# Performance work log

Hardware: AMD Instinct MI355X
Metric: run time of the kernel (lower is better)

Reference implementation:

```python
import jax, jax.numpy as jnp
import numpy as np

GROUP_SIZE = 128  # infeatures // n_groups = 4096 // 32


def setup_inputs() -> dict:
    key = jax.random.key(0)
    k1, k2, k3, k4 = jax.random.split(key, 4)
    M, K, N = 256, 4096, 4096
    n_groups = K // GROUP_SIZE  # 32
    A = jax.random.normal(k1, (M, K), dtype=jnp.float32)
    # uint4 quantized weights, stored unpacked as int32 in [0, 16)
    qweight = jax.random.randint(k2, (N, K), 0, 16, dtype=jnp.int32)
    scales = jax.random.uniform(k3, (N, n_groups), dtype=jnp.float32) * 0.05 + 1e-3
    zeros = jax.random.uniform(k4, (N, n_groups), dtype=jnp.float32) * 15.0
    return {"A": A, "qweight": qweight, "scales": scales, "zeros": zeros}


def reference(A, qweight, scales, zeros):
    # Fused dequant + GEMM: W[n,k] = (q[n,k] - zeros[n, k//G]) * scales[n, k//G]
    N, K = qweight.shape
    s = jnp.repeat(scales, GROUP_SIZE, axis=1)   # [N, K]
    z = jnp.repeat(zeros, GROUP_SIZE, axis=1)    # [N, K]
    W = (qweight.astype(A.dtype) - z) * s        # dequantized weight [N, K]
    # Linear: Y = A @ W^T  -> [M, N]
    return jnp.einsum('mk,nk->mn', A, W)
```

## Files before the change

### kernel.cpp

```cpp
#include <hip/hip_runtime.h>

typedef __attribute__((ext_vector_type(8))) short bf16x8;
typedef __attribute__((ext_vector_type(4))) float f32x4;

#define MDIM 256
#define NDIM 4096
#define KDIM 4096
#define NGRP 32
#define BM 128
#define BN 32
#define BK 64
#define NT (KDIM / BK)

typedef const __attribute__((address_space(1))) void* gas_ptr;
typedef __attribute__((address_space(3))) void* las_ptr;

__device__ __forceinline__ unsigned short f2bf(float f) {
  union { float f; unsigned int u; } v;
  v.f = f;
  unsigned int r = v.u + 0x7FFFu + ((v.u >> 16) & 1u);
  return (unsigned short)(r >> 16);
}

__device__ __forceinline__ void gl_lds16(const void* g, void* l) {
  __builtin_amdgcn_global_load_lds((gas_ptr)g, (las_ptr)l, 16, 0, 0);
}

__global__ void convA_kernel(const float* __restrict__ A,
                             unsigned short* __restrict__ Ab) {
  int i = blockIdx.x * 256 + threadIdx.x;
  float4 v = reinterpret_cast<const float4*>(A)[i];
  ushort4 o;
  o.x = f2bf(v.x); o.y = f2bf(v.y); o.z = f2bf(v.z); o.w = f2bf(v.w);
  reinterpret_cast<ushort4*>(Ab)[i] = o;
}

__global__ __launch_bounds__(256, 1) void gemm_kernel(
    const unsigned short* __restrict__ Ab, const int* __restrict__ qw,
    const float* __restrict__ sc, const float* __restrict__ zr,
    float* __restrict__ out) {
  __shared__ __align__(16) unsigned short A_lds[4][BM * BK];
  __shared__ __align__(16) unsigned short W_lds[2][BN * BK];
  __shared__ float s_lds[BN * NGRP];
  __shared__ float zs_lds[BN * NGRP];

  const int tid = threadIdx.x;
  const int lane = tid & 63;
  const int wave = tid >> 6;
  const int wm = wave >> 1;
  const int wn = wave & 1;

  const int bid = blockIdx.x;
  const int swz = (bid & 7) * 32 + (bid >> 3);
  const int m0 = (swz & 1) * BM;
  const int n0 = (swz >> 1) * BN;

  for (int i = tid; i < BN * NGRP; i += 256) {
    int n = i >> 5;
    int g = i & 31;
    float s = sc[(size_t)(n0 + n) * NGRP + g];
    float z = zr[(size_t)(n0 + n) * NGRP + g];
    s_lds[i] = s;
    zs_lds[i] = z * s;
  }

  const unsigned short* Abase = Ab + (size_t)m0 * KDIM;
  const int wrow = tid >> 3;
  const int wc = tid & 7;
  const int* qbase = qw + (size_t)(n0 + wrow) * KDIM + wc * 8;

  int4 qr[4][2];

  auto loadW = [&](int t, int idx) {
    const int* p = qbase + t * BK;
    qr[idx][0] = *reinterpret_cast<const int4*>(p);
    qr[idx][1] = *reinterpret_cast<const int4*>(p + 4);
  };
  auto stageA = [&](int t, int b) {
#pragma unroll
    for (int i = 0; i < 4; ++i) {
      int cid = i * 256 + tid;
      int row = cid >> 3;
      int cp = cid & 7;
      int cs = cp ^ (row & 7);
      const unsigned short* g = Abase + (size_t)row * KDIM + t * BK + cs * 8;
      gl_lds16(g, &A_lds[b][(i * 256 + wave * 64) * 8]);
    }
  };
  auto writeW = [&](int t, int b, int idx) {
    int gg = t >> 1;
    float s = s_lds[wrow * NGRP + gg];
    float zs = zs_lds[wrow * NGRP + gg];
    int q[8] = {qr[idx][0].x, qr[idx][0].y, qr[idx][0].z, qr[idx][0].w,
                qr[idx][1].x, qr[idx][1].y, qr[idx][1].z, qr[idx][1].w};
    bf16x8 w;
#pragma unroll
    for (int j = 0; j < 8; ++j)
      w[j] = (short)f2bf(fmaf((float)q[j], s, -zs));
    *reinterpret_cast<bf16x8*>(
        &W_lds[b][wrow * BK + ((wc ^ (wrow & 7)) << 3)]) = w;
  };

  f32x4 acc[4];
#pragma unroll
  for (int i = 0; i < 4; ++i) acc[i] = (f32x4){0.f, 0.f, 0.f, 0.f};

  const int l15 = lane & 15;
  const int lhi = lane >> 4;
  const int ar0 = wm * 64 + l15;
  const int asw = ar0 & 7;
  const int br = wn * 16 + l15;
  const int bsw = br & 7;

  auto compute = [&](int ab, int wb) {
#pragma unroll
    for (int ks = 0; ks < 2; ++ks) {
      bf16x8 bfr = *reinterpret_cast<const bf16x8*>(
          &W_lds[wb][br * BK + ((((ks << 2) + lhi) ^ bsw) << 3)]);
#pragma unroll
      for (int mi = 0; mi < 4; ++mi) {
        bf16x8 afr = *reinterpret_cast<const bf16x8*>(
            &A_lds[ab][(ar0 + mi * 16) * BK + ((((ks << 2) + lhi) ^ asw) << 3)]);
        acc[mi] = __builtin_amdgcn_mfma_f32_16x16x32_bf16(afr, bfr, acc[mi], 0, 0, 0);
      }
    }
  };

  loadW(0, 0); stageA(0, 0);
  loadW(1, 1); stageA(1, 1);
  loadW(2, 2); stageA(2, 2);

  asm volatile("s_waitcnt lgkmcnt(0)" ::: "memory");
  __builtin_amdgcn_s_barrier();
  __builtin_amdgcn_sched_barrier(0);
  writeW(0, 0, 0);
  asm volatile("s_waitcnt vmcnt(12) lgkmcnt(0)" ::: "memory");
  __builtin_amdgcn_s_barrier();
  __builtin_amdgcn_sched_barrier(0);

  for (int tb = 0; tb < NT; tb += 4) {
#pragma unroll
    for (int u = 0; u < 4; ++u) {
      const int t = tb + u;
      const int tp = (t + 3 < NT) ? (t + 3) : 0;
      loadW(tp, (u + 3) & 3);
      stageA(tp, (u + 3) & 3);
      compute(u, u & 1);
      if (t + 1 < NT) writeW(t + 1, (u + 1) & 1, (u + 1) & 3);
      asm volatile("s_waitcnt vmcnt(12) lgkmcnt(0)" ::: "memory");
      __builtin_amdgcn_s_barrier();
      __builtin_amdgcn_sched_barrier(0);
    }
  }

  const int col = n0 + wn * 16 + l15;
  const int rb = m0 + wm * 64 + (lhi << 2);
#pragma unroll
  for (int mi = 0; mi < 4; ++mi)
#pragma unroll
    for (int j = 0; j < 4; ++j)
      out[(size_t)(rb + mi * 16 + j) * NDIM + col] = acc[mi][j];
}

extern "C" void kernel_launch(void* const* d_in, const int* in_sizes, int n_in,
                              void* d_out, int out_size, void* d_ws, size_t ws_size,
                              hipStream_t stream) {
  const float* A = (const float*)d_in[0];
  const int* qw = (const int*)d_in[1];
  const float* sc = (const float*)d_in[2];
  const float* zr = (const float*)d_in[3];
  float* out = (float*)d_out;
  unsigned short* Ab = (unsigned short*)d_ws;

  convA_kernel<<<(MDIM * KDIM / 4) / 256, 256, 0, stream>>>(A, Ab);
  gemm_kernel<<<(MDIM / BM) * (NDIM / BN), 256, 0, stream>>>(Ab, qw, sc, zr, out);
}
```

Before: 141.6 us.

## Split K across two blocks with atomic accumulation into zeroed output

```diff
diff --git a/kernel.cpp b/kernel.cpp
--- a/kernel.cpp
+++ b/kernel.cpp
@@ -10,7 +10,9 @@
 #define BM 128
 #define BN 32
 #define BK 64
-#define NT (KDIM / BK)
+#define SPLITK 2
+#define KLOC (KDIM / SPLITK)
+#define NTL (KLOC / BK)
 
 typedef const __attribute__((address_space(1))) void* gas_ptr;
 typedef __attribute__((address_space(3))) void* las_ptr;
@@ -35,14 +37,14 @@
   reinterpret_cast<ushort4*>(Ab)[i] = o;
 }
 
-__global__ __launch_bounds__(256, 1) void gemm_kernel(
+__global__ __launch_bounds__(256, 2) void gemm_kernel(
     const unsigned short* __restrict__ Ab, const int* __restrict__ qw,
     const float* __restrict__ sc, const float* __restrict__ zr,
     float* __restrict__ out) {
   __shared__ __align__(16) unsigned short A_lds[4][BM * BK];
   __shared__ __align__(16) unsigned short W_lds[2][BN * BK];
-  __shared__ float s_lds[BN * NGRP];
-  __shared__ float zs_lds[BN * NGRP];
+  __shared__ float s_lds[BN * 16];
+  __shared__ float zs_lds[BN * 16];
 
   const int tid = threadIdx.x;
   const int lane = tid & 63;
@@ -51,23 +53,27 @@
   const int wn = wave & 1;
 
   const int bid = blockIdx.x;
-  const int swz = (bid & 7) * 32 + (bid >> 3);
-  const int m0 = (swz & 1) * BM;
-  const int n0 = (swz >> 1) * BN;
+  const int x = bid & 7;
+  const int j = bid >> 3;
+  const int r = x * 16 + (j >> 2);
+  const int c = j & 3;
+  const int m0 = (c & 1) * BM;
+  const int ks = c >> 1;
+  const int n0 = r * BN;
 
-  for (int i = tid; i < BN * NGRP; i += 256) {
-    int n = i >> 5;
-    int g = i & 31;
-    float s = sc[(size_t)(n0 + n) * NGRP + g];
-    float z = zr[(size_t)(n0 + n) * NGRP + g];
+  for (int i = tid; i < BN * 16; i += 256) {
+    int n = i >> 4;
+    int g16 = i & 15;
+    float s = sc[(size_t)(n0 + n) * NGRP + ks * 16 + g16];
+    float z = zr[(size_t)(n0 + n) * NGRP + ks * 16 + g16];
     s_lds[i] = s;
     zs_lds[i] = z * s;
   }
 
-  const unsigned short* Abase = Ab + (size_t)m0 * KDIM;
+  const unsigned short* Abase = Ab + (size_t)m0 * KDIM + ks * KLOC;
   const int wrow = tid >> 3;
   const int wc = tid & 7;
-  const int* qbase = qw + (size_t)(n0 + wrow) * KDIM + wc * 8;
+  const int* qbase = qw + (size_t)(n0 + wrow) * KDIM + ks * KLOC + wc * 8;
 
   int4 qr[4][2];
 
@@ -89,14 +95,14 @@
   };
   auto writeW = [&](int t, int b, int idx) {
     int gg = t >> 1;
-    float s = s_lds[wrow * NGRP + gg];
-    float zs = zs_lds[wrow * NGRP + gg];
+    float s = s_lds[wrow * 16 + gg];
+    float zs = zs_lds[wrow * 16 + gg];
     int q[8] = {qr[idx][0].x, qr[idx][0].y, qr[idx][0].z, qr[idx][0].w,
                 qr[idx][1].x, qr[idx][1].y, qr[idx][1].z, qr[idx][1].w};
     bf16x8 w;
 #pragma unroll
-    for (int j = 0; j < 8; ++j)
-      w[j] = (short)f2bf(fmaf((float)q[j], s, -zs));
+    for (int jj = 0; jj < 8; ++jj)
+      w[jj] = (short)f2bf(fmaf((float)q[jj], s, -zs));
     *reinterpret_cast<bf16x8*>(
         &W_lds[b][wrow * BK + ((wc ^ (wrow & 7)) << 3)]) = w;
   };
@@ -114,13 +120,13 @@
 
   auto compute = [&](int ab, int wb) {
 #pragma unroll
-    for (int ks = 0; ks < 2; ++ks) {
+    for (int kss = 0; kss < 2; ++kss) {
       bf16x8 bfr = *reinterpret_cast<const bf16x8*>(
-          &W_lds[wb][br * BK + ((((ks << 2) + lhi) ^ bsw) << 3)]);
+          &W_lds[wb][br * BK + ((((kss << 2) + lhi) ^ bsw) << 3)]);
 #pragma unroll
       for (int mi = 0; mi < 4; ++mi) {
         bf16x8 afr = *reinterpret_cast<const bf16x8*>(
-            &A_lds[ab][(ar0 + mi * 16) * BK + ((((ks << 2) + lhi) ^ asw) << 3)]);
+            &A_lds[ab][(ar0 + mi * 16) * BK + ((((kss << 2) + lhi) ^ asw) << 3)]);
         acc[mi] = __builtin_amdgcn_mfma_f32_16x16x32_bf16(afr, bfr, acc[mi], 0, 0, 0);
       }
     }
@@ -138,15 +144,15 @@
   __builtin_amdgcn_s_barrier();
   __builtin_amdgcn_sched_barrier(0);
 
-  for (int tb = 0; tb < NT; tb += 4) {
+  for (int tb = 0; tb < NTL; tb += 4) {
 #pragma unroll
     for (int u = 0; u < 4; ++u) {
       const int t = tb + u;
-      const int tp = (t + 3 < NT) ? (t + 3) : 0;
+      const int tp = (t + 3 < NTL) ? (t + 3) : 0;
       loadW(tp, (u + 3) & 3);
       stageA(tp, (u + 3) & 3);
       compute(u, u & 1);
-      if (t + 1 < NT) writeW(t + 1, (u + 1) & 1, (u + 1) & 3);
+      if (t + 1 < NTL) writeW(t + 1, (u + 1) & 1, (u + 1) & 3);
       asm volatile("s_waitcnt vmcnt(12) lgkmcnt(0)" ::: "memory");
       __builtin_amdgcn_s_barrier();
       __builtin_amdgcn_sched_barrier(0);
@@ -158,8 +164,9 @@
 #pragma unroll
   for (int mi = 0; mi < 4; ++mi)
 #pragma unroll
-    for (int j = 0; j < 4; ++j)
-      out[(size_t)(rb + mi * 16 + j) * NDIM + col] = acc[mi][j];
+    for (int jj = 0; jj < 4; ++jj)
+      unsafeAtomicAdd(&out[(size_t)(rb + mi * 16 + jj) * NDIM + col],
+                      acc[mi][jj]);
 }
 
 extern "C" void kernel_launch(void* const* d_in, const int* in_sizes, int n_in,
@@ -172,6 +179,8 @@
   float* out = (float*)d_out;
   unsigned short* Ab = (unsigned short*)d_ws;
 
+  hipMemsetAsync(d_out, 0, (size_t)MDIM * NDIM * sizeof(float), stream);
   convA_kernel<<<(MDIM * KDIM / 4) / 256, 256, 0, stream>>>(A, Ab);
-  gemm_kernel<<<(MDIM / BM) * (NDIM / BN), 256, 0, stream>>>(Ab, qw, sc, zr, out);
+  gemm_kernel<<<(MDIM / BM) * (NDIM / BN) * SPLITK, 256, 0, stream>>>(
+      Ab, qw, sc, zr, out);
 }
```

Result: faster. 136.9 us (-3.3%).
